# Kernel tuning notes

Hardware: AMD Instinct MI355X
Metric: run time of the kernel (lower is better)

The kernel has to match this reference:

```python
import jax, jax.numpy as jnp
import numpy as np

B, N, H, F = 4, 256, 192, 64
SUP = 1.0  # ancestor_suppression_strength
EPS = 1e-6


def setup_inputs() -> dict:
    key = jax.random.key(0)
    ks = jax.random.split(key, 14)
    z = jax.random.normal(ks[0], (B, H), jnp.float32)
    # strictly-lower-triangular 0/1 parent (link) matrix: row t lists parents j < t
    tri = jnp.tril(jnp.ones((N, N), jnp.float32), -1)
    targets = (jax.random.uniform(ks[1], (B, N, N)) < 0.05).astype(jnp.float32) * tri

    def w(k, shape):
        fan_in = shape[0]
        return jax.random.normal(k, shape, jnp.float32) / jnp.sqrt(jnp.float32(fan_in))

    return {
        "z": z,
        "teacher_forcing_targets": targets,
        "W_init": w(ks[2], (H, H)), "b_init": jnp.zeros((H,), jnp.float32),
        "W_ih": w(ks[3], (H, 3 * H)), "W_hh": w(ks[4], (H, 3 * H)),
        "b_ih": jnp.zeros((3 * H,), jnp.float32), "b_hh": jnp.zeros((3 * H,), jnp.float32),
        "W1": w(ks[5], (3 * H, H)), "b1": jnp.zeros((H,), jnp.float32),
        "W2": w(ks[6], (H, 1)), "b2": jnp.zeros((1,), jnp.float32),
        "Wf": w(ks[7], (H, F)), "bf": jnp.zeros((F,), jnp.float32),
        "atom_count": N,
    }


def gru_cell(x, h, W_ih, W_hh, b_ih, b_hh):
    gx = x @ W_ih + b_ih
    gh = h @ W_hh + b_hh
    xr, xu, xn = jnp.split(gx, 3, axis=-1)
    hr, hu, hn = jnp.split(gh, 3, axis=-1)
    r = jax.nn.sigmoid(xr + hr)
    u = jax.nn.sigmoid(xu + hu)
    n = jnp.tanh(xn + r * hn)
    return (1.0 - u) * n + u * h


def reference(z, teacher_forcing_targets, W_init, b_init, W_ih, W_hh, b_ih, b_hh,
              W1, b1, W2, b2, Wf, bf, atom_count):
    b, n = teacher_forcing_targets.shape[0], teacher_forcing_targets.shape[1]
    h = z.shape[-1]
    idx = jnp.arange(n)

    # decoder_init: latent z -> hidden state of node 0
    h0 = jnp.tanh(z @ W_init + b_init)
    S0 = jnp.zeros((b, n, h), z.dtype).at[:, 0].set(h0)   # node states
    A0 = jnp.zeros((b, n, n), z.dtype)                    # ancestor indicator A[b,i,j]=1 iff j ancestor of i

    def step(carry, xs):
        S, A, ll = carry
        t, tgt = xs                                   # t scalar, tgt (B,N) = parents of node t
        mask = (idx < t).astype(S.dtype)              # existing nodes
        cnt = jnp.maximum(mask.sum(), 1.0)
        # mean-aggregation over existing node states -> GRU message
        m = (S * mask[None, :, None]).sum(axis=1) / cnt              # (B,H)
        h_prov = gru_cell(m, z, W_ih, W_hh, b_ih, b_hh)              # provisional state of new node
        # parent logits: MLP([h_new, h_existing, z]) per candidate parent
        feats = jnp.concatenate([
            jnp.broadcast_to(h_prov[:, None, :], S.shape), S,
            jnp.broadcast_to(z[:, None, :], S.shape)], axis=-1)      # (B,N,3H)
        logits = (jax.nn.relu(feats @ W1 + b1) @ W2 + b2)[..., 0]    # (B,N)
        # ancestor suppression: suppress j if j is already an ancestor of one of t's parents
        reach = jnp.einsum('bn,bnm->bm', tgt, A)
        anc = (reach > 0).astype(S.dtype)
        p = jax.nn.sigmoid(logits) * (1.0 - SUP * anc)
        p = jnp.clip(p, EPS, 1.0 - EPS)
        ll = ll + (mask[None, :] * (tgt * jnp.log(p) + (1.0 - tgt) * jnp.log1p(-p))).sum()
        # teacher forcing: commit parents, update new-node state from parent states
        deg = jnp.maximum(tgt.sum(axis=-1, keepdims=True), 1.0)
        msg = jnp.einsum('bn,bnh->bh', tgt, S) / deg
        h_new = gru_cell(msg, h_prov, W_ih, W_hh, b_ih, b_hh)
        S = jax.lax.dynamic_update_slice(S, h_new[:, None, :], (0, t, 0))
        row = jnp.minimum(tgt + anc, 1.0)             # ancestors(t) = parents U ancestors(parents)
        A = jax.lax.dynamic_update_slice(A, row[:, None, :], (0, t, 0))
        return (S, A, ll), None

    ts = jnp.arange(1, n)
    tgt_rows = jnp.swapaxes(teacher_forcing_targets[:, 1:, :], 0, 1)  # (N-1,B,N)
    (S, A, ll), _ = jax.lax.scan(step, (S0, A0, jnp.zeros((), z.dtype)), (ts, tgt_rows))

    L = teacher_forcing_targets            # teacher-forced link matrix
    node_features = S @ Wf + bf            # node_feature_decoder head
    return L, node_features, ll
```

## Files before the change

kernel.cpp:

```cpp
#include <hip/hip_runtime.h>
#include <stdint.h>

#define B_ 4
#define N_ 256
#define H_ 192
#define H3_ 576
#define F_ 64
#define SH_ 24
#define SC_ 72

#define H0_OFF   0u
#define ZC_OFF   1024u
#define HL_OFF   2048u
#define SL_OFF   395264u
#define AN_OFF   788480u
#define TG_OFF   796672u
#define PL_OFF   804864u
#define PC_OFF   870400u
#define DG_OFF   871424u
#define G_OFF    872448u
#define C_OFF    1069056u
#define CL_OFF   1265664u
#define CC_OFF   1331200u
#define XC_OFF   1332224u
#define FHL_OFF  1332288u
#define FSL_OFF  1725504u

#define AN64 (AN_OFF/2)
#define TG64 (TG_OFF/2)

#define NF_OUT 262144u
#define LL_OUT 327680u

__device__ __forceinline__ float sigm_(float x){ return 1.0f/(1.0f + __expf(-x)); }
__device__ __forceinline__ float tanh_(float x){
  float ax = fabsf(x);
  float e = __expf(-2.0f*ax);
  float t = (1.0f - e)/(1.0f + e);
  return x < 0.0f ? -t : t;
}

__device__ __forceinline__ void st_mall_(uint32_t* p, unsigned long long u){
  __hip_atomic_store((unsigned long long*)p, u, __ATOMIC_RELAXED, __HIP_MEMORY_SCOPE_AGENT);
}
__device__ __forceinline__ unsigned long long ld_mall_(const uint32_t* p){
  return __hip_atomic_load((const unsigned long long*)p, __ATOMIC_RELAXED, __HIP_MEMORY_SCOPE_AGENT);
}
__device__ __forceinline__ unsigned long long ld_l2_(const uint32_t* p){
  unsigned long long v;
  asm volatile("global_load_dwordx2 %0, %1, off sc0\n\ts_waitcnt vmcnt(0)"
               : "=v"(v) : "v"(p) : "memory");
  return v;
}
__device__ __forceinline__ void pub_(uint32_t* fp, uint32_t* mp, float v, uint32_t tag){
  unsigned long long u = ((unsigned long long)tag<<32) | (unsigned long long)__float_as_uint(v);
  __hip_atomic_store((unsigned long long*)fp, u, __ATOMIC_RELAXED, __HIP_MEMORY_SCOPE_WORKGROUP);
  st_mall_(mp, u);
}
__device__ __forceinline__ float pollH_(const uint32_t* fp, const uint32_t* mp, int fast, uint32_t tag){
  unsigned long long x = 0; int it = 0;
  for(;;){
    if (fast){
      x = ld_l2_(fp);
      if ((uint32_t)(x>>32) != tag && (((++it) & 1) != 0)){
        unsigned long long m = ld_mall_(mp);
        if ((uint32_t)(m>>32) == tag) x = m;
      }
    } else {
      x = ld_mall_(mp);
    }
    if (__all((int)((uint32_t)(x>>32) == tag))) break;
  }
  return __uint_as_float((uint32_t)x);
}

__global__ void __launch_bounds__(192) k_pre1(const float* __restrict__ z,
    const float* __restrict__ Winit, const float* __restrict__ binit,
    const float* __restrict__ W1, const float* __restrict__ b1,
    const float* __restrict__ tgt, float* ws, float* out)
{
  int bx = blockIdx.x, b = blockIdx.y, tid = threadIdx.x;
  if (bx == N_){
    __shared__ float zs[H_];
    zs[tid] = z[b*H_ + tid];
    __syncthreads();
    float a0=0.f, a1=0.f;
    for (int k=0;k<H_;k++){
      float zv = zs[k];
      a0 += zv * Winit[(size_t)k*H_ + tid];
      a1 += zv * W1[(size_t)(2*H_ + k)*H_ + tid];
    }
    ws[H0_OFF + b*H_ + tid] = tanh_(a0 + binit[tid]);
    ws[ZC_OFF + b*H_ + tid] = a1 + b1[tid];
    if (b==0 && tid==0) out[LL_OUT] = 0.0f;
    return;
  }
  if (tid >= 64) return;
  int t = bx, lane = tid;
  uint32_t* wsu = (uint32_t*)ws;
  unsigned long long* ws64 = (unsigned long long*)ws;
  const float* row = tgt + ((size_t)(b*N_) + t)*N_;
  uint8_t* pl = ((uint8_t*)&wsu[PL_OFF]) + (size_t)(b*N_ + t)*N_;
  int cnt = 0;
  #pragma unroll
  for (int m=0;m<4;m++){
    float v = row[m*64 + lane];
    bool p = (v != 0.0f);
    unsigned long long bw = __ballot(p);
    if (lane == 0) ws64[TG64 + (size_t)(b*N_+t)*4 + m] = bw;
    if (p){
      int pos = cnt + (int)__popcll(bw & ((1ULL<<lane)-1ULL));
      pl[pos] = (uint8_t)(m*64 + lane);
    }
    cnt += (int)__popcll(bw);
  }
  if (lane == 0){
    wsu[PC_OFF + b*N_ + t] = (uint32_t)cnt;
    ws[DG_OFF + b*N_ + t] = 1.0f / fmaxf((float)cnt, 1.0f);
  }
}

__global__ void __launch_bounds__(64) k_pre2(float* ws)
{
  int j = blockIdx.x, b = blockIdx.y, lane = threadIdx.x;
  uint32_t* wsu = (uint32_t*)ws;
  unsigned long long* ws64 = (unsigned long long*)ws;
  uint8_t* cl = ((uint8_t*)&wsu[CL_OFF]) + (size_t)(b*N_ + j)*N_;
  int w = j >> 6; int sb = j & 63;
  int cnt = 0;
  #pragma unroll
  for (int m=0;m<4;m++){
    int t = m*64 + lane;
    unsigned long long rowm = ws64[TG64 + (size_t)(b*N_+t)*4 + w];
    bool p = ((rowm >> sb) & 1ULL) != 0ULL;
    unsigned long long bw = __ballot(p);
    if (p){
      int pos = cnt + (int)__popcll(bw & ((1ULL<<lane)-1ULL));
      cl[pos] = (uint8_t)t;
    }
    cnt += (int)__popcll(bw);
  }
  if (lane == 0) wsu[CC_OFF + b*N_ + j] = (uint32_t)cnt;
}

__global__ void __launch_bounds__(512) k_pass1(const float* __restrict__ z,
    const float* __restrict__ Wih, const float* __restrict__ Whh,
    const float* __restrict__ bih_g, const float* __restrict__ bhh_g,
    float* ws)
{
  int bx = blockIdx.x;
  int b = bx & 7;
  if (b >= B_) return;
  int slice = bx >> 3;
  int tid = threadIdx.x;
  float* wsf = ws;
  uint32_t* wsu = (uint32_t*)ws;
  unsigned long long* ws64 = (unsigned long long*)ws;

  __shared__ __align__(16) float sruns[H_];
  __shared__ __align__(16) float sh[H_];
  __shared__ __align__(16) float sPS[N_*SC_];
  __shared__ __align__(16) float sdelta[2][SC_];
  __shared__ int sfast[8];
  __shared__ unsigned long long sAB[N_][4];
  __shared__ float sDG[N_], sTF1[N_], sTF2[N_];

  const int hh = tid >> 4;
  const int kc = tid & 15;
  const bool mv = (hh < 24);

  uint32_t xcc = (uint32_t)__builtin_amdgcn_s_getreg((31u<<11) | 20u) & 15u;
  if (tid == 0)
    __hip_atomic_store(&wsu[XC_OFF + b*16 + slice], 0xC0DE0000u | xcc,
                       __ATOMIC_RELAXED, __HIP_MEMORY_SCOPE_AGENT);
  if (tid < 64){
    uint32_t v = 0; int ok;
    do {
      v = (tid < 8) ? __hip_atomic_load(&wsu[XC_OFF + b*16 + tid],
              __ATOMIC_RELAXED, __HIP_MEMORY_SCOPE_AGENT) : 0xC0DE0000u;
      ok = (int)((v >> 16) == 0xC0DEu);
    } while (!__all(ok));
    if (tid < 8) sfast[tid] = ((v & 0xFFu) == xcc) ? 1 : 0;
  }

  for (int i = tid; i < N_; i += 512){
    sDG[i] = wsf[DG_OFF + b*N_ + i];
    float f1 = 0.f, f2 = 0.f;
    if (i >= 1){
      unsigned long long w1 = ws64[TG64 + (size_t)(b*N_+i)*4 + ((i-1)>>6)];
      f1 = (float)((w1 >> ((i-1)&63)) & 1ULL);
    }
    if (i >= 2){
      unsigned long long w2 = ws64[TG64 + (size_t)(b*N_+i)*4 + ((i-2)>>6)];
      f2 = (float)((w2 >> ((i-2)&63)) & 1ULL);
    }
    sTF1[i] = f1; sTF2[i] = f2;
  }

  float rwih[3][12], rwhh[3][12], rbih[3], rbhh[3], rghz[3];
  if (mv){
    #pragma unroll
    for (int g=0; g<3; g++){
      int col = g*H_ + slice*SH_ + hh;
      #pragma unroll
      for (int i=0;i<12;i++){
        rwih[g][i] = Wih[(size_t)(kc*12+i)*H3_ + col];
        rwhh[g][i] = Whh[(size_t)(kc*12+i)*H3_ + col];
      }
      rbih[g] = bih_g[col];
      rbhh[g] = bhh_g[col];
    }
    float a0=0.f,a1=0.f,a2=0.f;
    #pragma unroll
    for (int i=0;i<12;i++){
      float zv = z[b*H_ + kc*12 + i];
      a0 += zv*rwhh[0][i]; a1 += zv*rwhh[1][i]; a2 += zv*rwhh[2][i];
    }
    #pragma unroll
    for (int m=1;m<16;m<<=1){
      a0 += __shfl_xor(a0,m); a1 += __shfl_xor(a1,m); a2 += __shfl_xor(a2,m);
    }
    rghz[0]=a0+rbhh[0]; rghz[1]=a1+rbhh[1]; rghz[2]=a2+rbhh[2];
  }
  float zreg = mv ? z[b*H_ + slice*SH_ + hh] : 0.0f;
  for (int i = tid; i < N_*SC_; i += 512) sPS[i] = 0.0f;
  if (tid >= 384 && tid < 388) sAB[0][tid-384] = 0ULL;
  if (mv && kc == 0){
    float v = wsf[H0_OFF + b*H_ + slice*SH_ + hh];
    int e = slice*SH_ + hh;
    pub_(&wsu[FSL_OFF + (unsigned)(b*N_)*384u + 2u*e],
         &wsu[SL_OFF  + (unsigned)(b*N_)*384u + 2u*e], v, 1u);
  }
  __syncthreads();

  const int fastf = (tid < 192) ? sfast[tid/SH_] : 0;
  float rsum = 0.f;
  float qp0=0.f,qp1=0.f,qp2=0.f, dp0=0.f,dp1=0.f,dp2=0.f;

  for (int t=1; t<N_; t++){
    const uint32_t tagS = (uint32_t)t;
    const uint32_t tagH = (uint32_t)(t+1);
    if (tid < 192){
      float v = pollH_(&wsu[FSL_OFF + (unsigned)(b*N_+(t-1))*384u + 2u*(unsigned)tid],
                       &wsu[SL_OFF  + (unsigned)(b*N_+(t-1))*384u + 2u*(unsigned)tid],
                       fastf, tagS);
      rsum += v;
      sruns[tid] = rsum;
    }
    __syncthreads();
    float hp=0.f, a20=0.f, a21=0.f, a22=0.f;
    if (mv){
      float dginv = sDG[t], tf1 = sTF1[t], tf2 = sTF2[t];
      float x[12];
      *(float4*)&x[0] = *(float4*)&sruns[kc*12];
      *(float4*)&x[4] = *(float4*)&sruns[kc*12+4];
      *(float4*)&x[8] = *(float4*)&sruns[kc*12+8];
      float q0=0.f,q1=0.f,q2=0.f;
      #pragma unroll
      for (int i=0;i<12;i++){
        q0 += x[i]*rwih[0][i]; q1 += x[i]*rwih[1][i]; q2 += x[i]*rwih[2][i];
      }
      #pragma unroll
      for (int m=1;m<16;m<<=1){
        q0 += __shfl_xor(q0,m); q1 += __shfl_xor(q1,m); q2 += __shfl_xor(q2,m);
      }
      float d0=q0-qp0, d1=q1-qp1, d2=q2-qp2;
      qp0=q0; qp1=q1; qp2=q2;
      if (kc == 0){
        sdelta[t&1][0*SH_+hh]=d0; sdelta[t&1][1*SH_+hh]=d1; sdelta[t&1][2*SH_+hh]=d2;
      }
      float pv0 = sPS[t*SC_ + 0*SH_ + hh];
      float pv1 = sPS[t*SC_ + 1*SH_ + hh];
      float pv2 = sPS[t*SC_ + 2*SH_ + hh];
      a20 = (pv0 + tf1*d0 + tf2*dp0)*dginv + rbih[0];
      a21 = (pv1 + tf1*d1 + tf2*dp1)*dginv + rbih[1];
      a22 = (pv2 + tf1*d2 + tf2*dp2)*dginv + rbih[2];
      dp0=d0; dp1=d1; dp2=d2;
      float invt = 1.0f/(float)t;
      float a10 = q0*invt + rbih[0];
      float a11 = q1*invt + rbih[1];
      float a12 = q2*invt + rbih[2];
      float r = sigm_(a10 + rghz[0]);
      float u = sigm_(a11 + rghz[1]);
      float n = tanh_(a12 + r*rghz[2]);
      hp = (1.0f-u)*n + u*zreg;
      if (kc == 0){
        int e = slice*SH_ + hh;
        pub_(&wsu[FHL_OFF + (unsigned)(b*N_+t)*384u + 2u*e],
             &wsu[HL_OFF  + (unsigned)(b*N_+t)*384u + 2u*e], hp, tagH);
      }
      if (tid < 192){
        float hv = pollH_(&wsu[FHL_OFF + (unsigned)(b*N_+t)*384u + 2u*(unsigned)tid],
                          &wsu[HL_OFF  + (unsigned)(b*N_+t)*384u + 2u*(unsigned)tid],
                          fastf, tagH);
        sh[tid] = hv;
      }
    } else {
      int lane = tid - 384;
      if (lane < SC_){
        if (t >= 2){
          int node = t-2;
          int ccn = (int)wsu[CC_OFF + b*N_ + node];
          const uint8_t* cl = ((const uint8_t*)&wsu[CL_OFF]) + (size_t)(b*N_ + node)*N_;
          float dd = sdelta[(t-1)&1][lane];
          for (int i=0;i<ccn;i++){
            int tc = cl[i];
            if (tc > t) sPS[tc*SC_ + lane] += dd;
          }
        }
      } else if (lane < SC_+4){
        int w = lane - SC_;
        int npt = (int)wsu[PC_OFF + b*N_ + t];
        const uint8_t* pb = ((const uint8_t*)&wsu[PL_OFF]) + (size_t)(b*N_ + t)*N_;
        unsigned long long acc = 0ULL;
        for (int i=0;i<npt;i++) acc |= sAB[pb[i]][w];
        if (slice == 0) ws64[AN64 + (size_t)(b*N_+t)*4 + w] = acc;
        sAB[t][w] = acc | ws64[TG64 + (size_t)(b*N_+t)*4 + w];
      }
    }
    __syncthreads();
    if (mv){
      float x[12];
      *(float4*)&x[0] = *(float4*)&sh[kc*12];
      *(float4*)&x[4] = *(float4*)&sh[kc*12+4];
      *(float4*)&x[8] = *(float4*)&sh[kc*12+8];
      float y0=0.f,y1=0.f,y2=0.f;
      #pragma unroll
      for (int i=0;i<12;i++){
        y0 += x[i]*rwhh[0][i]; y1 += x[i]*rwhh[1][i]; y2 += x[i]*rwhh[2][i];
      }
      #pragma unroll
      for (int m=1;m<16;m<<=1){
        y0 += __shfl_xor(y0,m); y1 += __shfl_xor(y1,m); y2 += __shfl_xor(y2,m);
      }
      float r2 = sigm_(a20 + y0 + rbhh[0]);
      float u2 = sigm_(a21 + y1 + rbhh[1]);
      float n2 = tanh_(a22 + r2*(y2 + rbhh[2]));
      float hn = (1.0f-u2)*n2 + u2*hp;
      if (kc == 0){
        int e = slice*SH_ + hh;
        pub_(&wsu[FSL_OFF + (unsigned)(b*N_+t)*384u + 2u*e],
             &wsu[SL_OFF  + (unsigned)(b*N_+t)*384u + 2u*e], hn, tagH);
      }
    }
  }
}

__global__ void k_p2a(const float* __restrict__ W1, const float* __restrict__ Wf,
    const float* __restrict__ bf, float* ws, float* out)
{
  int j = blockIdx.x, b = blockIdx.y, tid = threadIdx.x;
  __shared__ float srow[H_], hrow[H_];
  __shared__ float nfp[3][F_];
  srow[tid] = ws[SL_OFF + (unsigned)(b*N_+j)*384u + 2u*tid];
  hrow[tid] = ws[HL_OFF + (unsigned)(b*N_+j)*384u + 2u*tid];
  __syncthreads();
  float accG = 0.f, accC = 0.f;
  for (int k=0;k<H_;k++){
    float sv = srow[k], hv = hrow[k];
    accG += sv * W1[(size_t)(H_+k)*H_ + tid];
    accC += hv * W1[(size_t)k*H_ + tid];
  }
  ws[G_OFF + ((size_t)b*H_ + tid)*N_ + j] = accG;
  ws[C_OFF + (size_t)(b*N_+j)*H_ + tid] = accC + ws[ZC_OFF + b*H_ + tid];
  int f = tid & 63, kp = tid >> 6;
  float a = 0.f;
  for (int i=0;i<64;i++){ int k = kp*64 + i; a += srow[k]*Wf[(size_t)k*F_ + f]; }
  nfp[kp][f] = a;
  __syncthreads();
  if (tid < F_) out[NF_OUT + (size_t)(b*N_+j)*F_ + tid] = nfp[0][tid]+nfp[1][tid]+nfp[2][tid] + bf[tid];
}

__global__ void __launch_bounds__(256) k_p2b(const float* __restrict__ W2,
    const float* __restrict__ b2p, float* ws, float* out)
{
  int t = blockIdx.x + 1, b = blockIdx.y;
  int tid = threadIdx.x; int lane = tid & 63; int wv = tid >> 6;
  __shared__ float cv[H_], w2s[H_];
  __shared__ float wsum[4];
  unsigned long long* ws64 = (unsigned long long*)ws;
  if (tid < H_){
    cv[tid] = ws[C_OFF + (size_t)(b*N_+t)*H_ + tid];
    w2s[tid] = W2[tid];
  }
  __syncthreads();
  float acc = 0.f;
  if (tid < t){
    const float* GT = ws + G_OFF + (size_t)b*H_*N_;
    float a = 0.f;
    for (int k=0;k<H_;k++) a += fmaxf(cv[k] + GT[(size_t)k*N_ + tid], 0.f) * w2s[k];
    float logit = a + b2p[0];
    float pp = 1.0f/(1.0f+__expf(-logit));
    unsigned long long an = ws64[AN64 + (size_t)(b*N_+t)*4 + (tid>>6)];
    unsigned long long tg = ws64[TG64 + (size_t)(b*N_+t)*4 + (tid>>6)];
    float anc = (float)((an >> (tid&63)) & 1ULL);
    pp = pp * (1.0f - anc);
    pp = fminf(fmaxf(pp, 1e-6f), 1.0f - 1e-6f);
    int tgb = (int)((tg >> (tid&63)) & 1ULL);
    acc = tgb ? logf(pp) : log1pf(-pp);
  }
  #pragma unroll
  for (int m=32;m>=1;m>>=1) acc += __shfl_xor(acc, m);
  if (lane == 0) wsum[wv] = acc;
  __syncthreads();
  if (tid == 0) atomicAdd(out + LL_OUT, wsum[0]+wsum[1]+wsum[2]+wsum[3]);
}

extern "C" void kernel_launch(void* const* d_in, const int* in_sizes, int n_in,
                              void* d_out, int out_size, void* d_ws, size_t ws_size,
                              hipStream_t stream) {
  (void)in_sizes; (void)n_in; (void)out_size; (void)ws_size;
  const float* z     = (const float*)d_in[0];
  const float* tgt   = (const float*)d_in[1];
  const float* Winit = (const float*)d_in[2];
  const float* binit = (const float*)d_in[3];
  const float* Wih   = (const float*)d_in[4];
  const float* Whh   = (const float*)d_in[5];
  const float* bih   = (const float*)d_in[6];
  const float* bhh   = (const float*)d_in[7];
  const float* W1    = (const float*)d_in[8];
  const float* b1    = (const float*)d_in[9];
  const float* W2    = (const float*)d_in[10];
  const float* b2    = (const float*)d_in[11];
  const float* Wf    = (const float*)d_in[12];
  const float* bf    = (const float*)d_in[13];
  float* out = (float*)d_out;
  float* ws  = (float*)d_ws;

  hipMemcpyAsync(d_out, d_in[1], (size_t)B_*N_*N_*sizeof(float), hipMemcpyDeviceToDevice, stream);

  k_pre1<<<dim3(N_+1, B_), dim3(192), 0, stream>>>(z, Winit, binit, W1, b1, tgt, ws, out);
  k_pre2<<<dim3(N_, B_), dim3(64), 0, stream>>>(ws);
  k_pass1<<<dim3(64), dim3(512), 0, stream>>>(z, Wih, Whh, bih, bhh, ws);
  k_p2a<<<dim3(N_, B_), dim3(H_), 0, stream>>>(W1, Wf, bf, ws, out);
  k_p2b<<<dim3(N_-1, B_), dim3(256), 0, stream>>>(W2, b2, ws, out);
}
```

Measured before the change: 960.2 us.

## Exchange per-slice partial Wih projections instead of hidden states, halving cross-block handshakes

The recurrent kernel now has each of the 8 slice blocks publish its partial Wih product (576 columns) from its own 24 new hidden values. Every block then polls and sums all 8 partials itself, so each step needs one cross-block exchange instead of two (no separate publish/poll of the provisional hidden state). The provisional GRU is computed redundantly in every block, and the z·Whh term moves into a new small pre-kernel. The XCC-aware fast-path polling is dropped, and k_p2a now handles 8 rows per block to reuse weight loads. The cost is more polling traffic per step (8 loads per thread) and duplicated work.

```diff
diff --git a/kernel.cpp b/kernel.cpp
--- a/kernel.cpp
+++ b/kernel.cpp
@@ -11,20 +11,19 @@
 
 #define H0_OFF   0u
 #define ZC_OFF   1024u
-#define HL_OFF   2048u
-#define SL_OFF   395264u
-#define AN_OFF   788480u
-#define TG_OFF   796672u
-#define PL_OFF   804864u
-#define PC_OFF   870400u
-#define DG_OFF   871424u
-#define G_OFF    872448u
-#define C_OFF    1069056u
-#define CL_OFF   1265664u
-#define CC_OFF   1331200u
-#define XC_OFF   1332224u
-#define FHL_OFF  1332288u
-#define FSL_OFF  1725504u
+#define GHZ_OFF  2048u
+#define SL2_OFF  8192u
+#define HL2_OFF  204800u
+#define AN_OFF   401408u
+#define TG_OFF   409600u
+#define PL_OFF   417792u
+#define PC_OFF   483328u
+#define DG_OFF   484352u
+#define CL_OFF   485376u
+#define CC_OFF   550912u
+#define PQ_OFF   551936u
+#define G_OFF    625664u
+#define C_OFF    822272u
 
 #define AN64 (AN_OFF/2)
 #define TG64 (TG_OFF/2)
@@ -40,38 +39,37 @@
   return x < 0.0f ? -t : t;
 }
 
-__device__ __forceinline__ void st_mall_(uint32_t* p, unsigned long long u){
-  __hip_atomic_store((unsigned long long*)p, u, __ATOMIC_RELAXED, __HIP_MEMORY_SCOPE_AGENT);
-}
-__device__ __forceinline__ unsigned long long ld_mall_(const uint32_t* p){
-  return __hip_atomic_load((const unsigned long long*)p, __ATOMIC_RELAXED, __HIP_MEMORY_SCOPE_AGENT);
-}
-__device__ __forceinline__ unsigned long long ld_l2_(const uint32_t* p){
-  unsigned long long v;
-  asm volatile("global_load_dwordx2 %0, %1, off sc0\n\ts_waitcnt vmcnt(0)"
-               : "=v"(v) : "v"(p) : "memory");
-  return v;
-}
-__device__ __forceinline__ void pub_(uint32_t* fp, uint32_t* mp, float v, uint32_t tag){
+__device__ __forceinline__ void stq_(unsigned long long* p, float v, uint32_t tag){
   unsigned long long u = ((unsigned long long)tag<<32) | (unsigned long long)__float_as_uint(v);
-  __hip_atomic_store((unsigned long long*)fp, u, __ATOMIC_RELAXED, __HIP_MEMORY_SCOPE_WORKGROUP);
-  st_mall_(mp, u);
-}
-__device__ __forceinline__ float pollH_(const uint32_t* fp, const uint32_t* mp, int fast, uint32_t tag){
-  unsigned long long x = 0; int it = 0;
+  __hip_atomic_store(p, u, __ATOMIC_RELAXED, __HIP_MEMORY_SCOPE_AGENT);
+}
+__device__ __forceinline__ float poll8_(const unsigned long long* base, uint32_t tag){
+  unsigned long long x[8];
   for(;;){
-    if (fast){
-      x = ld_l2_(fp);
-      if ((uint32_t)(x>>32) != tag && (((++it) & 1) != 0)){
-        unsigned long long m = ld_mall_(mp);
-        if ((uint32_t)(m>>32) == tag) x = m;
-      }
-    } else {
-      x = ld_mall_(mp);
-    }
-    if (__all((int)((uint32_t)(x>>32) == tag))) break;
-  }
-  return __uint_as_float((uint32_t)x);
+    #pragma unroll
+    for (int k=0;k<8;k++)
+      x[k] = __hip_atomic_load(base + (size_t)k*576, __ATOMIC_RELAXED, __HIP_MEMORY_SCOPE_AGENT);
+    bool ok = true;
+    #pragma unroll
+    for (int k=0;k<8;k++) ok &= ((uint32_t)(x[k]>>32) == tag);
+    if (__all((int)ok)) break;
+  }
+  float s = 0.f;
+  #pragma unroll
+  for (int k=0;k<8;k++) s += __uint_as_float((uint32_t)x[k]);
+  return s;
+}
+
+__global__ void __launch_bounds__(576) k_pre0(const float* __restrict__ z,
+    const float* __restrict__ Whh, const float* __restrict__ bhh, float* ws)
+{
+  int b = blockIdx.x, tid = threadIdx.x;
+  __shared__ float sz[H_];
+  if (tid < H_) sz[tid] = z[b*H_ + tid];
+  __syncthreads();
+  float acc = 0.f;
+  for (int k=0;k<H_;k++) acc += sz[k] * Whh[(size_t)k*H3_ + tid];
+  ws[GHZ_OFF + b*H3_ + tid] = acc + bhh[tid];
 }
 
 __global__ void __launch_bounds__(192) k_pre1(const float* __restrict__ z,
@@ -143,7 +141,7 @@
   if (lane == 0) wsu[CC_OFF + b*N_ + j] = (uint32_t)cnt;
 }
 
-__global__ void __launch_bounds__(512) k_pass1(const float* __restrict__ z,
+__global__ void __launch_bounds__(576) k_pass1(const float* __restrict__ z,
     const float* __restrict__ Wih, const float* __restrict__ Whh,
     const float* __restrict__ bih_g, const float* __restrict__ bhh_g,
     float* ws)
@@ -156,34 +154,40 @@
   float* wsf = ws;
   uint32_t* wsu = (uint32_t*)ws;
   unsigned long long* ws64 = (unsigned long long*)ws;
-
-  __shared__ __align__(16) float sruns[H_];
-  __shared__ __align__(16) float sh[H_];
+  unsigned long long* PQ = (unsigned long long*)&wsu[PQ_OFF];
+
   __shared__ __align__(16) float sPS[N_*SC_];
-  __shared__ __align__(16) float sdelta[2][SC_];
-  __shared__ int sfast[8];
+  __shared__ __align__(16) float sq[H3_];
+  __shared__ __align__(16) float sdelta[2][H3_];
+  __shared__ __align__(16) float shp[H_];
+  __shared__ __align__(16) float sh_new[SH_];
+  __shared__ __align__(16) float sghz[H3_], sbih[H3_], sbhh[H3_];
+  __shared__ __align__(16) float sz[H_];
   __shared__ unsigned long long sAB[N_][4];
   __shared__ float sDG[N_], sTF1[N_], sTF2[N_];
 
-  const int hh = tid >> 4;
-  const int kc = tid & 15;
-  const bool mv = (hh < 24);
-
-  uint32_t xcc = (uint32_t)__builtin_amdgcn_s_getreg((31u<<11) | 20u) & 15u;
-  if (tid == 0)
-    __hip_atomic_store(&wsu[XC_OFF + b*16 + slice], 0xC0DE0000u | xcc,
-                       __ATOMIC_RELAXED, __HIP_MEMORY_SCOPE_AGENT);
-  if (tid < 64){
-    uint32_t v = 0; int ok;
-    do {
-      v = (tid < 8) ? __hip_atomic_load(&wsu[XC_OFF + b*16 + tid],
-              __ATOMIC_RELAXED, __HIP_MEMORY_SCOPE_AGENT) : 0xC0DE0000u;
-      ok = (int)((v >> 16) == 0xC0DEu);
-    } while (!__all(ok));
-    if (tid < 8) sfast[tid] = ((v & 0xFFu) == xcc) ? 1 : 0;
-  }
-
-  for (int i = tid; i < N_; i += 512){
+  float rwih[SH_];
+  #pragma unroll
+  for (int i=0;i<SH_;i++) rwih[i] = Wih[(size_t)(slice*SH_+i)*H3_ + tid];
+  const int h2 = tid >> 4, kc = tid & 15;
+  const bool mv2 = (tid < 384);
+  float rwhh[3][12];
+  if (mv2){
+    #pragma unroll
+    for (int g=0; g<3; g++){
+      int col = g*H_ + slice*SH_ + h2;
+      #pragma unroll
+      for (int i=0;i<12;i++) rwhh[g][i] = Whh[(size_t)(kc*12+i)*H3_ + col];
+    }
+  }
+
+  sbih[tid] = bih_g[tid];
+  sbhh[tid] = bhh_g[tid];
+  sghz[tid] = wsf[GHZ_OFF + b*H3_ + tid];
+  if (tid < H_) sz[tid] = z[b*H_ + tid];
+  for (int i = tid; i < N_*SC_; i += 576) sPS[i] = 0.0f;
+  if (tid < 4) sAB[0][tid] = 0ULL;
+  for (int i = tid; i < N_; i += 576){
     sDG[i] = wsf[DG_OFF + b*N_ + i];
     float f1 = 0.f, f2 = 0.f;
     if (i >= 1){
@@ -196,134 +200,70 @@
     }
     sTF1[i] = f1; sTF2[i] = f2;
   }
-
-  float rwih[3][12], rwhh[3][12], rbih[3], rbhh[3], rghz[3];
-  if (mv){
-    #pragma unroll
-    for (int g=0; g<3; g++){
-      int col = g*H_ + slice*SH_ + hh;
+  float h0s[SH_];
+  #pragma unroll
+  for (int i=0;i<SH_;i++) h0s[i] = wsf[H0_OFF + b*H_ + slice*SH_ + i];
+  if (tid >= slice*SH_ && tid < slice*SH_+SH_)
+    wsf[SL2_OFF + (unsigned)(b*N_)*192u + tid] = h0s[tid - slice*SH_];
+  {
+    float pc = 0.f;
+    #pragma unroll
+    for (int i=0;i<SH_;i++) pc += h0s[i]*rwih[i];
+    stq_(&PQ[((size_t)(1*4 + b)*8 + slice)*576 + tid], pc, 1u);
+  }
+  __syncthreads();
+
+  float qc = 0.f;
+
+  for (int t=1; t<N_; t++){
+    const uint32_t tag = (uint32_t)t;
+    {
+      float d = poll8_(&PQ[((size_t)((t&1)*4 + b)*8 + 0)*576 + tid], tag);
+      qc += d;
+      sq[tid] = qc;
+      sdelta[t&1][tid] = d;
+    }
+    __syncthreads();
+    if (tid < H_){
+      float invt = 1.0f/(float)t;
+      float a10 = sq[tid]*invt       + sbih[tid];
+      float a11 = sq[H_+tid]*invt    + sbih[H_+tid];
+      float a12 = sq[2*H_+tid]*invt  + sbih[2*H_+tid];
+      float r = sigm_(a10 + sghz[tid]);
+      float u = sigm_(a11 + sghz[H_+tid]);
+      float n = tanh_(a12 + r*sghz[2*H_+tid]);
+      float hp = (1.0f-u)*n + u*sz[tid];
+      shp[tid] = hp;
+      if (tid >= slice*SH_ && tid < slice*SH_+SH_)
+        wsf[HL2_OFF + (unsigned)(b*N_+t)*192u + tid] = hp;
+    } else if (tid >= 384 && tid < 384+SC_){
+      if (t >= 2){
+        int cc = tid - 384;
+        int g = cc/SH_, hcol = cc%SH_;
+        int gcol = g*H_ + slice*SH_ + hcol;
+        int node = t-2;
+        int ccn = (int)wsu[CC_OFF + b*N_ + node];
+        const uint8_t* cl = ((const uint8_t*)&wsu[CL_OFF]) + (size_t)(b*N_ + node)*N_;
+        float dd = sdelta[(t-1)&1][gcol];
+        for (int i=0;i<ccn;i++){
+          int tc = cl[i];
+          if (tc > t) sPS[tc*SC_ + cc] += dd;
+        }
+      }
+    } else if (tid >= 456 && tid < 460){
+      int w = tid - 456;
+      int npt = (int)wsu[PC_OFF + b*N_ + t];
+      const uint8_t* pb = ((const uint8_t*)&wsu[PL_OFF]) + (size_t)(b*N_ + t)*N_;
+      unsigned long long acc = 0ULL;
+      for (int i=0;i<npt;i++) acc |= sAB[pb[i]][w];
+      if (slice == 0) ws64[AN64 + (size_t)(b*N_+t)*4 + w] = acc;
+      sAB[t][w] = acc | ws64[TG64 + (size_t)(b*N_+t)*4 + w];
+    }
+    __syncthreads();
+    if (mv2){
+      float x[12];
       #pragma unroll
-      for (int i=0;i<12;i++){
-        rwih[g][i] = Wih[(size_t)(kc*12+i)*H3_ + col];
-        rwhh[g][i] = Whh[(size_t)(kc*12+i)*H3_ + col];
-      }
-      rbih[g] = bih_g[col];
-      rbhh[g] = bhh_g[col];
-    }
-    float a0=0.f,a1=0.f,a2=0.f;
-    #pragma unroll
-    for (int i=0;i<12;i++){
-      float zv = z[b*H_ + kc*12 + i];
-      a0 += zv*rwhh[0][i]; a1 += zv*rwhh[1][i]; a2 += zv*rwhh[2][i];
-    }
-    #pragma unroll
-    for (int m=1;m<16;m<<=1){
-      a0 += __shfl_xor(a0,m); a1 += __shfl_xor(a1,m); a2 += __shfl_xor(a2,m);
-    }
-    rghz[0]=a0+rbhh[0]; rghz[1]=a1+rbhh[1]; rghz[2]=a2+rbhh[2];
-  }
-  float zreg = mv ? z[b*H_ + slice*SH_ + hh] : 0.0f;
-  for (int i = tid; i < N_*SC_; i += 512) sPS[i] = 0.0f;
-  if (tid >= 384 && tid < 388) sAB[0][tid-384] = 0ULL;
-  if (mv && kc == 0){
-    float v = wsf[H0_OFF + b*H_ + slice*SH_ + hh];
-    int e = slice*SH_ + hh;
-    pub_(&wsu[FSL_OFF + (unsigned)(b*N_)*384u + 2u*e],
-         &wsu[SL_OFF  + (unsigned)(b*N_)*384u + 2u*e], v, 1u);
-  }
-  __syncthreads();
-
-  const int fastf = (tid < 192) ? sfast[tid/SH_] : 0;
-  float rsum = 0.f;
-  float qp0=0.f,qp1=0.f,qp2=0.f, dp0=0.f,dp1=0.f,dp2=0.f;
-
-  for (int t=1; t<N_; t++){
-    const uint32_t tagS = (uint32_t)t;
-    const uint32_t tagH = (uint32_t)(t+1);
-    if (tid < 192){
-      float v = pollH_(&wsu[FSL_OFF + (unsigned)(b*N_+(t-1))*384u + 2u*(unsigned)tid],
-                       &wsu[SL_OFF  + (unsigned)(b*N_+(t-1))*384u + 2u*(unsigned)tid],
-                       fastf, tagS);
-      rsum += v;
-      sruns[tid] = rsum;
-    }
-    __syncthreads();
-    float hp=0.f, a20=0.f, a21=0.f, a22=0.f;
-    if (mv){
-      float dginv = sDG[t], tf1 = sTF1[t], tf2 = sTF2[t];
-      float x[12];
-      *(float4*)&x[0] = *(float4*)&sruns[kc*12];
-      *(float4*)&x[4] = *(float4*)&sruns[kc*12+4];
-      *(float4*)&x[8] = *(float4*)&sruns[kc*12+8];
-      float q0=0.f,q1=0.f,q2=0.f;
-      #pragma unroll
-      for (int i=0;i<12;i++){
-        q0 += x[i]*rwih[0][i]; q1 += x[i]*rwih[1][i]; q2 += x[i]*rwih[2][i];
-      }
-      #pragma unroll
-      for (int m=1;m<16;m<<=1){
-        q0 += __shfl_xor(q0,m); q1 += __shfl_xor(q1,m); q2 += __shfl_xor(q2,m);
-      }
-      float d0=q0-qp0, d1=q1-qp1, d2=q2-qp2;
-      qp0=q0; qp1=q1; qp2=q2;
-      if (kc == 0){
-        sdelta[t&1][0*SH_+hh]=d0; sdelta[t&1][1*SH_+hh]=d1; sdelta[t&1][2*SH_+hh]=d2;
-      }
-      float pv0 = sPS[t*SC_ + 0*SH_ + hh];
-      float pv1 = sPS[t*SC_ + 1*SH_ + hh];
-      float pv2 = sPS[t*SC_ + 2*SH_ + hh];
-      a20 = (pv0 + tf1*d0 + tf2*dp0)*dginv + rbih[0];
-      a21 = (pv1 + tf1*d1 + tf2*dp1)*dginv + rbih[1];
-      a22 = (pv2 + tf1*d2 + tf2*dp2)*dginv + rbih[2];
-      dp0=d0; dp1=d1; dp2=d2;
-      float invt = 1.0f/(float)t;
-      float a10 = q0*invt + rbih[0];
-      float a11 = q1*invt + rbih[1];
-      float a12 = q2*invt + rbih[2];
-      float r = sigm_(a10 + rghz[0]);
-      float u = sigm_(a11 + rghz[1]);
-      float n = tanh_(a12 + r*rghz[2]);
-      hp = (1.0f-u)*n + u*zreg;
-      if (kc == 0){
-        int e = slice*SH_ + hh;
-        pub_(&wsu[FHL_OFF + (unsigned)(b*N_+t)*384u + 2u*e],
-             &wsu[HL_OFF  + (unsigned)(b*N_+t)*384u + 2u*e], hp, tagH);
-      }
-      if (tid < 192){
-        float hv = pollH_(&wsu[FHL_OFF + (unsigned)(b*N_+t)*384u + 2u*(unsigned)tid],
-                          &wsu[HL_OFF  + (unsigned)(b*N_+t)*384u + 2u*(unsigned)tid],
-                          fastf, tagH);
-        sh[tid] = hv;
-      }
-    } else {
-      int lane = tid - 384;
-      if (lane < SC_){
-        if (t >= 2){
-          int node = t-2;
-          int ccn = (int)wsu[CC_OFF + b*N_ + node];
-          const uint8_t* cl = ((const uint8_t*)&wsu[CL_OFF]) + (size_t)(b*N_ + node)*N_;
-          float dd = sdelta[(t-1)&1][lane];
-          for (int i=0;i<ccn;i++){
-            int tc = cl[i];
-            if (tc > t) sPS[tc*SC_ + lane] += dd;
-          }
-        }
-      } else if (lane < SC_+4){
-        int w = lane - SC_;
-        int npt = (int)wsu[PC_OFF + b*N_ + t];
-        const uint8_t* pb = ((const uint8_t*)&wsu[PL_OFF]) + (size_t)(b*N_ + t)*N_;
-        unsigned long long acc = 0ULL;
-        for (int i=0;i<npt;i++) acc |= sAB[pb[i]][w];
-        if (slice == 0) ws64[AN64 + (size_t)(b*N_+t)*4 + w] = acc;
-        sAB[t][w] = acc | ws64[TG64 + (size_t)(b*N_+t)*4 + w];
-      }
-    }
-    __syncthreads();
-    if (mv){
-      float x[12];
-      *(float4*)&x[0] = *(float4*)&sh[kc*12];
-      *(float4*)&x[4] = *(float4*)&sh[kc*12+4];
-      *(float4*)&x[8] = *(float4*)&sh[kc*12+8];
+      for (int i=0;i<12;i++) x[i] = shp[kc*12 + i];
       float y0=0.f,y1=0.f,y2=0.f;
       #pragma unroll
       for (int i=0;i<12;i++){
@@ -333,42 +273,80 @@
       for (int m=1;m<16;m<<=1){
         y0 += __shfl_xor(y0,m); y1 += __shfl_xor(y1,m); y2 += __shfl_xor(y2,m);
       }
-      float r2 = sigm_(a20 + y0 + rbhh[0]);
-      float u2 = sigm_(a21 + y1 + rbhh[1]);
-      float n2 = tanh_(a22 + r2*(y2 + rbhh[2]));
-      float hn = (1.0f-u2)*n2 + u2*hp;
+      float dginv = sDG[t], tf1 = sTF1[t], tf2 = sTF2[t];
+      int c0g = 0*H_ + slice*SH_ + h2;
+      int c1g = 1*H_ + slice*SH_ + h2;
+      int c2g = 2*H_ + slice*SH_ + h2;
+      float a20 = (sPS[t*SC_ + 0*SH_ + h2] + tf1*sdelta[t&1][c0g] + tf2*sdelta[(t-1)&1][c0g])*dginv + sbih[c0g];
+      float a21 = (sPS[t*SC_ + 1*SH_ + h2] + tf1*sdelta[t&1][c1g] + tf2*sdelta[(t-1)&1][c1g])*dginv + sbih[c1g];
+      float a22 = (sPS[t*SC_ + 2*SH_ + h2] + tf1*sdelta[t&1][c2g] + tf2*sdelta[(t-1)&1][c2g])*dginv + sbih[c2g];
+      float r2 = sigm_(a20 + y0 + sbhh[c0g]);
+      float u2 = sigm_(a21 + y1 + sbhh[c1g]);
+      float n2 = tanh_(a22 + r2*(y2 + sbhh[c2g]));
+      float hn = (1.0f-u2)*n2 + u2*shp[slice*SH_ + h2];
       if (kc == 0){
-        int e = slice*SH_ + hh;
-        pub_(&wsu[FSL_OFF + (unsigned)(b*N_+t)*384u + 2u*e],
-             &wsu[SL_OFF  + (unsigned)(b*N_+t)*384u + 2u*e], hn, tagH);
+        sh_new[h2] = hn;
+        wsf[SL2_OFF + (unsigned)(b*N_+t)*192u + slice*SH_ + h2] = hn;
       }
     }
-  }
-}
-
-__global__ void k_p2a(const float* __restrict__ W1, const float* __restrict__ Wf,
-    const float* __restrict__ bf, float* ws, float* out)
-{
-  int j = blockIdx.x, b = blockIdx.y, tid = threadIdx.x;
-  __shared__ float srow[H_], hrow[H_];
-  __shared__ float nfp[3][F_];
-  srow[tid] = ws[SL_OFF + (unsigned)(b*N_+j)*384u + 2u*tid];
-  hrow[tid] = ws[HL_OFF + (unsigned)(b*N_+j)*384u + 2u*tid];
-  __syncthreads();
-  float accG = 0.f, accC = 0.f;
+    __syncthreads();
+    {
+      float pc = 0.f;
+      #pragma unroll
+      for (int i=0;i<SH_;i++) pc += sh_new[i]*rwih[i];
+      stq_(&PQ[((size_t)(((t+1)&1)*4 + b)*8 + slice)*576 + tid], pc, (uint32_t)(t+1));
+    }
+    __syncthreads();
+  }
+}
+
+__global__ void __launch_bounds__(192) k_p2a(const float* __restrict__ W1,
+    const float* __restrict__ Wf, const float* __restrict__ bf, float* ws, float* out)
+{
+  int j0 = blockIdx.x * 8, b = blockIdx.y, tid = threadIdx.x;
+  __shared__ float srow[8][H_], hrow[8][H_];
+  __shared__ float nfp[3][8][F_];
+  for (int r=0;r<8;r++){
+    srow[r][tid] = ws[SL2_OFF + (unsigned)(b*N_+j0+r)*192u + tid];
+    hrow[r][tid] = ws[HL2_OFF + (unsigned)(b*N_+j0+r)*192u + tid];
+  }
+  __syncthreads();
+  float accG[8], accC[8];
+  #pragma unroll
+  for (int r=0;r<8;r++){ accG[r]=0.f; accC[r]=0.f; }
   for (int k=0;k<H_;k++){
-    float sv = srow[k], hv = hrow[k];
-    accG += sv * W1[(size_t)(H_+k)*H_ + tid];
-    accC += hv * W1[(size_t)k*H_ + tid];
-  }
-  ws[G_OFF + ((size_t)b*H_ + tid)*N_ + j] = accG;
-  ws[C_OFF + (size_t)(b*N_+j)*H_ + tid] = accC + ws[ZC_OFF + b*H_ + tid];
+    float w1a = W1[(size_t)k*H_ + tid];
+    float w1b = W1[(size_t)(H_+k)*H_ + tid];
+    #pragma unroll
+    for (int r=0;r<8;r++){
+      accG[r] += srow[r][k]*w1b;
+      accC[r] += hrow[r][k]*w1a;
+    }
+  }
+  float zc = ws[ZC_OFF + b*H_ + tid];
+  #pragma unroll
+  for (int r=0;r<8;r++){
+    ws[G_OFF + ((size_t)b*H_ + tid)*N_ + j0 + r] = accG[r];
+    ws[C_OFF + (size_t)(b*N_+j0+r)*H_ + tid] = accC[r] + zc;
+  }
   int f = tid & 63, kp = tid >> 6;
-  float a = 0.f;
-  for (int i=0;i<64;i++){ int k = kp*64 + i; a += srow[k]*Wf[(size_t)k*F_ + f]; }
-  nfp[kp][f] = a;
-  __syncthreads();
-  if (tid < F_) out[NF_OUT + (size_t)(b*N_+j)*F_ + tid] = nfp[0][tid]+nfp[1][tid]+nfp[2][tid] + bf[tid];
+  float acc[8];
+  #pragma unroll
+  for (int r=0;r<8;r++) acc[r] = 0.f;
+  for (int i=0;i<64;i++){
+    int k = kp*64 + i;
+    float wfv = Wf[(size_t)k*F_ + f];
+    #pragma unroll
+    for (int r=0;r<8;r++) acc[r] += srow[r][k]*wfv;
+  }
+  #pragma unroll
+  for (int r=0;r<8;r++) nfp[kp][r][f] = acc[r];
+  __syncthreads();
+  if (tid < F_){
+    #pragma unroll
+    for (int r=0;r<8;r++)
+      out[NF_OUT + (size_t)(b*N_+j0+r)*F_ + tid] = nfp[0][r][tid]+nfp[1][r][tid]+nfp[2][r][tid] + bf[tid];
+  }
 }
 
 __global__ void __launch_bounds__(256) k_p2b(const float* __restrict__ W2,
@@ -429,9 +407,10 @@
 
   hipMemcpyAsync(d_out, d_in[1], (size_t)B_*N_*N_*sizeof(float), hipMemcpyDeviceToDevice, stream);
 
+  k_pre0<<<dim3(B_), dim3(H3_), 0, stream>>>(z, Whh, bhh, ws);
   k_pre1<<<dim3(N_+1, B_), dim3(192), 0, stream>>>(z, Winit, binit, W1, b1, tgt, ws, out);
   k_pre2<<<dim3(N_, B_), dim3(64), 0, stream>>>(ws);
-  k_pass1<<<dim3(64), dim3(512), 0, stream>>>(z, Wih, Whh, bih, bhh, ws);
-  k_p2a<<<dim3(N_, B_), dim3(H_), 0, stream>>>(W1, Wf, bf, ws, out);
+  k_pass1<<<dim3(64), dim3(H3_), 0, stream>>>(z, Wih, Whh, bih, bhh, ws);
+  k_p2a<<<dim3(N_/8, B_), dim3(192), 0, stream>>>(W1, Wf, bf, ws, out);
   k_p2b<<<dim3(N_-1, B_), dim3(256), 0, stream>>>(W2, b2, ws, out);
 }
```

After: 1.139 ms. 1.19x slower.
